# Kernel optimization log

Measured on AMD Instinct MI355X. Metric: run time of the kernel, lower is better.

## Reference

```python
import jax, jax.numpy as jnp
import numpy as np

# CTC-CRF constants (bonito defaults): state_len=5, alphabet='NACGT' -> n_base=4
STATE_LEN = 5
N_BASE = 4
S = N_BASE ** STATE_LEN          # 1024 states
NZ = N_BASE + 1                  # 5 incoming transitions per state (stay + 4 moves)
C = S * NZ                       # 5120 score channels per timestep


def _make_idx():
    # idx[s] = indices into alpha (previous states) feeding state s.
    # Matches torch: cat([arange(S)[:,None], arange(S).repeat_interleave(n_base).reshape(n_base,-1).T], 1)
    a = np.arange(S)
    idx = np.concatenate([a[:, None], np.repeat(a, N_BASE).reshape(N_BASE, S).T], axis=1)
    return jnp.asarray(idx, dtype=jnp.int32)  # [S, NZ]


def setup_inputs() -> dict:
    key = jax.random.key(0)
    T, N = 2000, 32
    scores = jax.random.normal(key, (T, N, C), dtype=jnp.float32)
    return {"scores": scores}


def reference(scores) -> jnp.ndarray:
    # Faithful jax version of CTC_CRF.logZ(scores) with the Log semiring:
    #   alpha[t+1] = logsumexp(Ms[t] + alpha[t][:, idx], axis=-1)
    #   logZ = logsumexp(alpha[T] + vT, axis=1)
    T, N, _ = scores.shape
    idx = _make_idx()                      # [S, NZ] int32
    Ms = scores.reshape(T, N, S, NZ)       # [T, N, S, NZ]
    v0 = jnp.zeros((N, S), dtype=scores.dtype)  # semiring one = 0.0
    vT = jnp.zeros((N, S), dtype=scores.dtype)

    def step(alpha, Ms_t):
        # alpha: [N, S]; gather predecessors -> [N, S, NZ]; semiring mul = add; sum = logsumexp
        a_next = jax.nn.logsumexp(Ms_t + alpha[:, idx], axis=-1)
        return a_next, None

    alpha_T, _ = jax.lax.scan(step, v0, Ms)
    return jax.nn.logsumexp(alpha_T + vT, axis=1)  # [N]
```

## Files before the change

### kernel.cpp

```cpp
#include <hip/hip_runtime.h>
#include <cstdint>
#include <cstddef>


#define NB 32
#define SD 1024
#define CD 5120

typedef float f4a __attribute__((ext_vector_type(4), aligned(4)));

__device__ __forceinline__ float fexp2(float x) { return __builtin_amdgcn_exp2f(x); }
__device__ __forceinline__ float flog2(float x) { return __builtin_amdgcn_logf(x); }

__global__ void __launch_bounds__(1024) ctc_logz(const float* __restrict__ scores,
                                                 float* __restrict__ out, int T) {
  __shared__ float ap[2 * SD];
  __shared__ float red[32];

  const int tid = threadIdx.x;
  const int n = blockIdx.x;
  const int lane = tid & 63;
  const int wid = tid >> 6;
  const int p4 = (tid >> 2) << 2;
  const int awr = ((tid & 255) << 2) | (tid >> 8);

  ap[tid] = 0.f;
  ap[SD + tid] = 0.f;
  float a_cur = 0.f;

  const float K = 1.44269504088896340736f;
  const float LN2 = 0.69314718055994530942f;

  const float* sn = scores + (size_t)n * CD + (size_t)tid * 5;
  const size_t tstr = (size_t)NB * CD;
  const size_t str8 = 8 * tstr;

  auto CP = [&](int t, const f4a& qa, float qb) {
    const f4a av = *(const f4a*)&ap[((t + 1) & 1) * SD + p4];
    float t0 = qa.x + a_cur;
    float t1 = qa.y + av.x;
    float t2 = qa.z + av.y;
    float t3 = qa.w + av.z;
    float t4 = qb + av.w;
    float mx = fmaxf(t4, fmaxf(fmaxf(t0, t1), fmaxf(t2, t3)));
    float nk = -mx * K;
    float s = fexp2(__builtin_fmaf(t0, K, nk));
    s += fexp2(__builtin_fmaf(t1, K, nk));
    s += fexp2(__builtin_fmaf(t2, K, nk));
    s += fexp2(__builtin_fmaf(t3, K, nk));
    s += fexp2(__builtin_fmaf(t4, K, nk));
    a_cur = __builtin_fmaf(flog2(s), LN2, mx);
    ap[(t & 1) * SD + awr] = a_cur;
    asm volatile("s_waitcnt lgkmcnt(0)\n\ts_barrier" ::: "memory");
  };

#define PRO(c)                                                              \
  const float* P##c = sn + (size_t)((c) < T ? (c) : T - 1) * tstr;          \
  f4a qa##c = *(const f4a*)P##c;                                            \
  float qb##c = P##c[4];                                                    \
  P##c += str8;
  PRO(0) PRO(1) PRO(2) PRO(3) PRO(4) PRO(5) PRO(6) PRO(7)
#undef PRO

  __syncthreads();

#define RL(c)                                                               \
  qa##c = *(const f4a*)P##c;                                                \
  qb##c = P##c[4];                                                          \
  P##c += str8;

  int t = 0;
  for (; t + 16 <= T; t += 8) {
    CP(t + 0, qa0, qb0); RL(0)
    CP(t + 1, qa1, qb1); RL(1)
    CP(t + 2, qa2, qb2); RL(2)
    CP(t + 3, qa3, qb3); RL(3)
    CP(t + 4, qa4, qb4); RL(4)
    CP(t + 5, qa5, qb5); RL(5)
    CP(t + 6, qa6, qb6); RL(6)
    CP(t + 7, qa7, qb7); RL(7)
  }
#undef RL

#define EPI1(c)                                                             \
  if (t + (c) < T) {                                                        \
    CP(t + (c), qa##c, qb##c);                                              \
    if (t + 8 + (c) < T) { qa##c = *(const f4a*)P##c; qb##c = P##c[4]; }    \
  }
  EPI1(0) EPI1(1) EPI1(2) EPI1(3) EPI1(4) EPI1(5) EPI1(6) EPI1(7)
#undef EPI1
  t += 8;
#define EPI2(c) if (t + (c) < T) CP(t + (c), qa##c, qb##c);
  EPI2(0) EPI2(1) EPI2(2) EPI2(3) EPI2(4) EPI2(5) EPI2(6) EPI2(7)
#undef EPI2

  float m = a_cur;
#pragma unroll
  for (int d = 1; d < 64; d <<= 1) m = fmaxf(m, __shfl_xor(m, d, 64));
  if (lane == 0) red[wid] = m;
  __syncthreads();
  float bm = red[0];
#pragma unroll
  for (int i = 1; i < 16; ++i) bm = fmaxf(bm, red[i]);
  float e = fexp2((a_cur - bm) * K);
#pragma unroll
  for (int d = 1; d < 64; d <<= 1) e += __shfl_xor(e, d, 64);
  if (lane == 0) red[16 + wid] = e;
  __syncthreads();
  if (tid == 0) {
    float ssum = red[16];
#pragma unroll
    for (int i = 1; i < 16; ++i) ssum += red[16 + i];
    out[n] = __builtin_fmaf(flog2(ssum), LN2, bm);
  }
}

extern "C" void kernel_launch(void* const* d_in, const int* in_sizes, int n_in,
                              void* d_out, int out_size, void* d_ws, size_t ws_size,
                              hipStream_t stream) {
  const float* scores = (const float*)d_in[0];
  float* out = (float*)d_out;
  const long long tot = (long long)in_sizes[0];
  const int T = (int)(tot / ((long long)NB * CD));
  ctc_logz<<<dim3(NB), dim3(1024), 0, stream>>>(scores, out, T);
}
```

Before: 771.3 us.

## Run CRF forward recursion in linear space with power-of-two rescaling

```diff
diff --git a/kernel.cpp b/kernel.cpp
--- a/kernel.cpp
+++ b/kernel.cpp
@@ -15,7 +15,7 @@
 __global__ void __launch_bounds__(1024) ctc_logz(const float* __restrict__ scores,
                                                  float* __restrict__ out, int T) {
   __shared__ float ap[2 * SD];
-  __shared__ float red[32];
+  __shared__ float red[16];
 
   const int tid = threadIdx.x;
   const int n = blockIdx.x;
@@ -24,9 +24,10 @@
   const int p4 = (tid >> 2) << 2;
   const int awr = ((tid & 255) << 2) | (tid >> 8);
 
-  ap[tid] = 0.f;
-  ap[SD + tid] = 0.f;
-  float a_cur = 0.f;
+  ap[tid] = 1.f;
+  ap[SD + tid] = 1.f;
+  float a_cur = 1.f;
+  int cacc = 0;
 
   const float K = 1.44269504088896340736f;
   const float LN2 = 0.69314718055994530942f;
@@ -36,21 +37,24 @@
   const size_t str8 = 8 * tstr;
 
   auto CP = [&](int t, const f4a& qa, float qb) {
-    const f4a av = *(const f4a*)&ap[((t + 1) & 1) * SD + p4];
-    float t0 = qa.x + a_cur;
-    float t1 = qa.y + av.x;
-    float t2 = qa.z + av.y;
-    float t3 = qa.w + av.z;
-    float t4 = qb + av.w;
-    float mx = fmaxf(t4, fmaxf(fmaxf(t0, t1), fmaxf(t2, t3)));
-    float nk = -mx * K;
-    float s = fexp2(__builtin_fmaf(t0, K, nk));
-    s += fexp2(__builtin_fmaf(t1, K, nk));
-    s += fexp2(__builtin_fmaf(t2, K, nk));
-    s += fexp2(__builtin_fmaf(t3, K, nk));
-    s += fexp2(__builtin_fmaf(t4, K, nk));
-    a_cur = __builtin_fmaf(flog2(s), LN2, mx);
-    ap[(t & 1) * SD + awr] = a_cur;
+    const int rbuf = ((t + 1) & 1) * SD;
+    const f4a av = *(const f4a*)&ap[rbuf + p4];
+    const float R = ap[rbuf];
+    const int xb = (__float_as_int(R) >> 23) & 0xFF;
+    cacc += xb;
+    const float nLf = (float)(127 - xb);
+    float e0 = fexp2(__builtin_fmaf(qa.x, K, nLf));
+    float e1 = fexp2(__builtin_fmaf(qa.y, K, nLf));
+    float e2 = fexp2(__builtin_fmaf(qa.z, K, nLf));
+    float e3 = fexp2(__builtin_fmaf(qa.w, K, nLf));
+    float e4 = fexp2(__builtin_fmaf(qb,   K, nLf));
+    float s = e0 * a_cur;
+    s = __builtin_fmaf(e1, av.x, s);
+    s = __builtin_fmaf(e2, av.y, s);
+    s = __builtin_fmaf(e3, av.z, s);
+    s = __builtin_fmaf(e4, av.w, s);
+    a_cur = s;
+    ap[(t & 1) * SD + awr] = s;
     asm volatile("s_waitcnt lgkmcnt(0)\n\ts_barrier" ::: "memory");
   };
 
@@ -94,24 +98,16 @@
   EPI2(0) EPI2(1) EPI2(2) EPI2(3) EPI2(4) EPI2(5) EPI2(6) EPI2(7)
 #undef EPI2
 
-  float m = a_cur;
+  float v = a_cur;
 #pragma unroll
-  for (int d = 1; d < 64; d <<= 1) m = fmaxf(m, __shfl_xor(m, d, 64));
-  if (lane == 0) red[wid] = m;
-  __syncthreads();
-  float bm = red[0];
-#pragma unroll
-  for (int i = 1; i < 16; ++i) bm = fmaxf(bm, red[i]);
-  float e = fexp2((a_cur - bm) * K);
-#pragma unroll
-  for (int d = 1; d < 64; d <<= 1) e += __shfl_xor(e, d, 64);
-  if (lane == 0) red[16 + wid] = e;
+  for (int d = 1; d < 64; d <<= 1) v += __shfl_xor(v, d, 64);
+  if (lane == 0) red[wid] = v;
   __syncthreads();
   if (tid == 0) {
-    float ssum = red[16];
+    float ssum = red[0];
 #pragma unroll
-    for (int i = 1; i < 16; ++i) ssum += red[16 + i];
-    out[n] = __builtin_fmaf(flog2(ssum), LN2, bm);
+    for (int i = 1; i < 16; ++i) ssum += red[i];
+    out[n] = LN2 * ((float)(cacc - 127 * T) + flog2(ssum));
   }
 }
 
```

Result: no change. 761.8 us (-1.2%).
